# Optimization experiments

Hardware: AMD Instinct MI355X
Metric: run time of the kernel (lower is better)

Reference implementation:

```python
import jax, jax.numpy as jnp
import numpy as np

D_MODEL = 512
N_HEADS = 8
D_HEAD = D_MODEL // N_HEADS
D_FF = 2048
LN_EPS = 1e-5


def _layer_norm(x, g, b):
    mu = jnp.mean(x, axis=-1, keepdims=True)
    var = jnp.var(x, axis=-1, keepdims=True)
    return (x - mu) * jax.lax.rsqrt(var + LN_EPS) * g + b


def setup_inputs() -> dict:
    key = jax.random.key(0)
    ks = jax.random.split(key, 16)
    s_d = 1.0 / np.sqrt(D_MODEL)
    s_f = 1.0 / np.sqrt(D_FF)
    x = jax.random.normal(ks[0], (32, 512, D_MODEL), dtype=jnp.float32)
    # per-head Q/K/V linears stacked over heads: [H, D, dh] weights, [H, dh] biases
    Wq = jax.random.uniform(ks[1], (N_HEADS, D_MODEL, D_HEAD), jnp.float32, -s_d, s_d)
    bq = jax.random.uniform(ks[2], (N_HEADS, D_HEAD), jnp.float32, -s_d, s_d)
    Wk = jax.random.uniform(ks[3], (N_HEADS, D_MODEL, D_HEAD), jnp.float32, -s_d, s_d)
    bk = jax.random.uniform(ks[4], (N_HEADS, D_HEAD), jnp.float32, -s_d, s_d)
    Wv = jax.random.uniform(ks[5], (N_HEADS, D_MODEL, D_HEAD), jnp.float32, -s_d, s_d)
    bv = jax.random.uniform(ks[6], (N_HEADS, D_HEAD), jnp.float32, -s_d, s_d)
    Wo = jax.random.uniform(ks[7], (D_MODEL, D_MODEL), jnp.float32, -s_d, s_d)
    bo = jax.random.uniform(ks[8], (D_MODEL,), jnp.float32, -s_d, s_d)
    ln1_g = jnp.ones((D_MODEL,), jnp.float32)
    ln1_b = jnp.zeros((D_MODEL,), jnp.float32)
    W1 = jax.random.uniform(ks[9], (D_MODEL, D_FF), jnp.float32, -s_d, s_d)
    b1 = jax.random.uniform(ks[10], (D_FF,), jnp.float32, -s_d, s_d)
    W2 = jax.random.uniform(ks[11], (D_FF, D_MODEL), jnp.float32, -s_f, s_f)
    b2 = jax.random.uniform(ks[12], (D_MODEL,), jnp.float32, -s_f, s_f)
    ln2_g = jnp.ones((D_MODEL,), jnp.float32)
    ln2_b = jnp.zeros((D_MODEL,), jnp.float32)
    return dict(x=x, Wq=Wq, bq=bq, Wk=Wk, bk=bk, Wv=Wv, bv=bv, Wo=Wo, bo=bo,
                ln1_g=ln1_g, ln1_b=ln1_b, W1=W1, b1=b1, W2=W2, b2=b2,
                ln2_g=ln2_g, ln2_b=ln2_b)


def reference(x, Wq, bq, Wk, bk, Wv, bv, Wo, bo, ln1_g, ln1_b, W1, b1, W2, b2, ln2_g, ln2_b):
    B, T, D = x.shape
    # batched-heads Q/K/V: [B, H, T, dh]
    q = jnp.einsum('btd,hde->bhte', x, Wq) + bq[None, :, None, :]
    k = jnp.einsum('btd,hde->bhte', x, Wk) + bk[None, :, None, :]
    v = jnp.einsum('btd,hde->bhte', x, Wv) + bv[None, :, None, :]
    scale = D_HEAD ** -0.5
    scores = jnp.einsum('bhte,bhse->bhts', q, k) * scale  # [B,H,T,T]
    causal = jnp.tril(jnp.ones((T, T), dtype=bool))
    scores = jnp.where(causal[None, None], scores, -jnp.inf)
    w = jax.nn.softmax(scores, axis=-1)
    o = jnp.einsum('bhts,bhse->bhte', w, v)              # [B,H,T,dh]
    o = jnp.transpose(o, (0, 2, 1, 3)).reshape(B, T, D)   # concat heads
    attn = o @ Wo + bo
    out1 = x + _layer_norm(attn, ln1_g, ln1_b)            # post-LN on sublayer output (as in source)
    ff = jax.nn.relu(out1 @ W1 + b1) @ W2 + b2
    return out1 + _layer_norm(ff, ln2_g, ln2_b)
```

## Files before the change

### kernel.cpp

```cpp
#include <hip/hip_runtime.h>
#include <hip/hip_bf16.h>


#define D_MODEL 512
#define N_HEADS 8
#define D_HEAD 64
#define D_FF 2048
#define NROWS 16384

typedef __bf16 bf16x8 __attribute__((ext_vector_type(8)));
typedef float f32x4 __attribute__((ext_vector_type(4)));
typedef float f32x16 __attribute__((ext_vector_type(16)));

#define SWZ(x) ((x) ^ ((((x) >> 7) & 7) << 4))

static __device__ __forceinline__ ushort f2bf(float f) {
    union { float f; unsigned u; } v; v.f = f;
    unsigned r = v.u + 0x7fffu + ((v.u >> 16) & 1u);
    return (ushort)(r >> 16);
}
static __device__ __forceinline__ unsigned pack2(float lo, float hi) {
    return (unsigned)f2bf(lo) | ((unsigned)f2bf(hi) << 16);
}
static __device__ __forceinline__ float bf2f(ushort u) {
    union { unsigned u; float f; } v; v.u = (unsigned)u << 16;
    return v.f;
}
static __device__ __forceinline__ void async16(const void* g, void* l) {
    __builtin_amdgcn_global_load_lds(
        (const __attribute__((address_space(1))) void*)g,
        (__attribute__((address_space(3))) void*)l, 16, 0, 0);
}

static __device__ __forceinline__ void tile_transpose_body(
    const float* __restrict__ src, int srcldc, ushort* __restrict__ dst, int Rd,
    int r0, int c0)
{
    __shared__ float t[64][65];
    int tid = threadIdx.x;
    int lr = tid >> 4, lc4 = (tid & 15) * 4;
    #pragma unroll
    for (int i = 0; i < 4; ++i) {
        float4 v = *(const float4*)&src[(size_t)(r0 + lr + i * 16) * srcldc + c0 + lc4];
        t[lr + i * 16][lc4 + 0] = v.x;
        t[lr + i * 16][lc4 + 1] = v.y;
        t[lr + i * 16][lc4 + 2] = v.z;
        t[lr + i * 16][lc4 + 3] = v.w;
    }
    __syncthreads();
    int oc = tid >> 2, orr = (tid & 3) * 16;
    uint4 u0, u1;
    u0.x = pack2(t[orr + 0][oc],  t[orr + 1][oc]);
    u0.y = pack2(t[orr + 2][oc],  t[orr + 3][oc]);
    u0.z = pack2(t[orr + 4][oc],  t[orr + 5][oc]);
    u0.w = pack2(t[orr + 6][oc],  t[orr + 7][oc]);
    u1.x = pack2(t[orr + 8][oc],  t[orr + 9][oc]);
    u1.y = pack2(t[orr + 10][oc], t[orr + 11][oc]);
    u1.z = pack2(t[orr + 12][oc], t[orr + 13][oc]);
    u1.w = pack2(t[orr + 14][oc], t[orr + 15][oc]);
    ushort* d = dst + (size_t)(c0 + oc) * Rd + r0 + orr;
    *(uint4*)&d[0] = u0;
    *(uint4*)&d[8] = u1;
}

__global__ __launch_bounds__(256) void prep_kernel(
    const float* __restrict__ x, ushort* __restrict__ x_bf,
    const float* __restrict__ Wq, const float* __restrict__ Wk,
    const float* __restrict__ Wv, ushort* __restrict__ WpT,
    const float* __restrict__ Wo, ushort* __restrict__ WoT,
    const float* __restrict__ W1, ushort* __restrict__ W1T,
    const float* __restrict__ W2, ushort* __restrict__ W2T,
    const float* __restrict__ bq, const float* __restrict__ bk,
    const float* __restrict__ bv, float* __restrict__ bp)
{
    const int blk = blockIdx.x;
    const int tid = threadIdx.x;
    if (blk < 4096) {
        int i = blk * 256 + tid;
        const float4* s = (const float4*)x;
        float4 a = s[i * 2], b = s[i * 2 + 1];
        uint4 o;
        o.x = pack2(a.x, a.y); o.y = pack2(a.z, a.w);
        o.z = pack2(b.x, b.y); o.w = pack2(b.z, b.w);
        ((uint4*)x_bf)[i] = o;
    } else if (blk < 4288) {
        int idx = blk - 4096;
        int z = idx >> 3, y = idx & 7;
        int p = z >> 3, h = z & 7;
        const float* src = ((p == 0) ? Wq : (p == 1) ? Wk : Wv) +
                           (size_t)h * D_MODEL * D_HEAD;
        ushort* dst = WpT + (size_t)(p * D_MODEL + h * D_HEAD) * D_MODEL;
        tile_transpose_body(src, D_HEAD, dst, D_MODEL, y * 64, 0);
    } else if (blk < 4352) {
        int idx = blk - 4288;
        tile_transpose_body(Wo, 512, WoT, 512, (idx >> 3) * 64, (idx & 7) * 64);
    } else if (blk < 4608) {
        int idx = blk - 4352;
        tile_transpose_body(W1, 2048, W1T, 512, (idx >> 5) * 64, (idx & 31) * 64);
    } else if (blk < 4864) {
        int idx = blk - 4608;
        tile_transpose_body(W2, 512, W2T, 2048, (idx >> 3) * 64, (idx & 7) * 64);
    } else {
        int gid = (blk - 4864) * 256 + tid;
        if (gid < 3 * D_MODEL) {
            int p = gid / D_MODEL;
            int h = (gid % D_MODEL) / D_HEAD;
            int e = gid % D_HEAD;
            const float* bb = (p == 0) ? bq : (p == 1) ? bk : bv;
            bp[gid] = bb[h * D_HEAD + e];
        }
    }
}

template<int OMODE, bool RELU>
__global__ __launch_bounds__(512, 1) void gemm_bf16_kernel(
    const ushort* __restrict__ A, const ushort* __restrict__ BT,
    const float* __restrict__ bias, void* __restrict__ Cout,
    ushort* __restrict__ Qg, ushort* __restrict__ Kg, ushort* __restrict__ Vt,
    int M, int N, int K, int nbx)
{
    extern __shared__ __align__(16) char smem[];

    const int tid = threadIdx.x;
    const int wid = tid >> 6, l = tid & 63;
    const int wr = wid >> 1, wc = wid & 1;

    const int cpx = gridDim.x >> 3;
    const int flat = blockIdx.x;
    const int swz = (flat & 7) * cpx + (flat >> 3);
    const int bx = swz % nbx, by = swz / nbx;
    const int m0 = by * 256, n0 = bx * 128;

    const int srow = tid >> 3;
    const int sbyte = (tid & 7) * 16;
    const int ssw = sbyte ^ ((srow & 7) << 4);

    #define STAGE(t)                                                          \
    {                                                                         \
        const int kk_ = (t) * 64;                                             \
        char* dst_ = smem + ((t) & 1) * 49152;                                \
        _Pragma("unroll")                                                     \
        for (int i = 0; i < 4; ++i)                                           \
            async16((const char*)(A + (size_t)(m0 + i * 64 + srow) * K + kk_) \
                        + ssw,                                                \
                    dst_ + i * 8192 + tid * 16);                              \
        _Pragma("unroll")                                                     \
        for (int i = 0; i < 2; ++i)                                           \
            async16((const char*)(BT + (size_t)(n0 + i * 64 + srow) * K + kk_)\
                        + ssw,                                                \
                    dst_ + 32768 + i * 8192 + tid * 16);                      \
    }

    const int fl = l & 31, fh = l >> 5;
    const int frsw = (fl & 7) << 4;

    f32x16 acc[2][2] = {};

    const int T = K >> 6;
    STAGE(0);
    asm volatile("s_waitcnt vmcnt(0)" ::: "memory");
    __builtin_amdgcn_s_barrier();
    __builtin_amdgcn_sched_barrier(0);

    for (int t = 0; t < T; ++t) {
        if (t + 1 < T) STAGE(t + 1);

        const char* bufA = smem + (t & 1) * 49152;
        const char* bufB = bufA + 32768;
        #pragma unroll
        for (int ks = 0; ks < 4; ++ks) {
            const int kb = ((ks * 32 + fh * 16) ^ frsw);
            bf16x8 af[2], bfv[2];
            #pragma unroll
            for (int mi = 0; mi < 2; ++mi)
                af[mi] = *(const bf16x8*)(bufA +
                    (wr * 64 + mi * 32 + fl) * 128 + kb);
            #pragma unroll
            for (int ni = 0; ni < 2; ++ni)
                bfv[ni] = *(const bf16x8*)(bufB +
                    (wc * 64 + ni * 32 + fl) * 128 + kb);
            #pragma unroll
            for (int mi = 0; mi < 2; ++mi)
                #pragma unroll
                for (int ni = 0; ni < 2; ++ni)
                    acc[mi][ni] = __builtin_amdgcn_mfma_f32_32x32x16_bf16(
                        af[mi], bfv[ni], acc[mi][ni], 0, 0, 0);
        }

        if (t + 1 < T) {
            asm volatile("s_waitcnt vmcnt(0)" ::: "memory");
            __builtin_amdgcn_s_barrier();
            __builtin_amdgcn_sched_barrier(0);
        }
    }
    #undef STAGE

    #pragma unroll
    for (int ni = 0; ni < 2; ++ni) {
        const int c = n0 + wc * 64 + ni * 32 + fl;
        const float bvv = bias ? bias[c] : 0.f;
        #pragma unroll
        for (int mi = 0; mi < 2; ++mi) {
            const int rbase = m0 + wr * 64 + mi * 32 + (fh << 2);
            float vv[16];
            #pragma unroll
            for (int reg = 0; reg < 16; ++reg) {
                float v = acc[mi][ni][reg] + bvv;
                if (RELU) v = fmaxf(v, 0.f);
                vv[reg] = v;
            }
            if (OMODE == 1) {
                #pragma unroll
                for (int reg = 0; reg < 16; ++reg) {
                    int r = rbase + (reg & 3) + ((reg >> 2) << 3);
                    ((ushort*)Cout)[(size_t)r * N + c] = f2bf(vv[reg]);
                }
            } else {
                const int p = n0 >> 9;
                const int h = (c >> 6) & 7, e = c & 63;
                #pragma unroll
                for (int q = 0; q < 4; ++q) {
                    int r0 = rbase + (q << 3);
                    int b = r0 >> 9, t0 = r0 & 511;
                    size_t bh = (size_t)(b * 8 + h);
                    if (p == 2) {
                        uint2 pk;
                        pk.x = pack2(vv[q * 4 + 0], vv[q * 4 + 1]);
                        pk.y = pack2(vv[q * 4 + 2], vv[q * 4 + 3]);
                        *(uint2*)&Vt[bh * 32768 + (size_t)e * 512 + t0] = pk;
                    } else {
                        ushort* dst = (p == 0 ? Qg : Kg) + bh * 32768 +
                                      (size_t)t0 * 64 + e;
                        dst[0]   = f2bf(vv[q * 4 + 0]);
                        dst[64]  = f2bf(vv[q * 4 + 1]);
                        dst[128] = f2bf(vv[q * 4 + 2]);
                        dst[192] = f2bf(vv[q * 4 + 3]);
                    }
                }
            }
        }
    }
}

__global__ __launch_bounds__(256) void attn_kernel(
    const ushort* __restrict__ Qg,
    const ushort* __restrict__ Kg,
    const ushort* __restrict__ Vt,
    ushort* __restrict__ O)
{
    __shared__ __align__(16) char QP[8192];
    __shared__ __align__(16) char KB[2][8192];
    __shared__ __align__(16) char VB[2][8192];

    const int bh = blockIdx.x, qb = blockIdx.y;
    const int tid = threadIdx.x;
    const int w = tid >> 6, l = tid & 63;

    const ushort* Qb = Qg + (size_t)bh * 32768;
    const ushort* Kb = Kg + (size_t)bh * 32768;
    const ushort* Vb = Vt + (size_t)bh * 32768;

    #pragma unroll
    for (int i = 0; i < 2; ++i) {
        int Xi = i * 4096 + tid * 16;
        int row = Xi >> 7;
        int sw = SWZ(Xi) & 127;
        async16((const char*)(Qb + (size_t)(qb * 64 + row) * 64) + sw, QP + Xi);
    }
    #define STAGEKV(kt, bb)                                                     \
        { _Pragma("unroll")                                                     \
          for (int i = 0; i < 2; ++i) {                                         \
              int Xi = i * 4096 + tid * 16;                                     \
              int row = Xi >> 7;                                                \
              int sw = SWZ(Xi) & 127;                                           \
              async16((const char*)(Kb + (size_t)((kt) * 64 + row) * 64) + sw,  \
                      KB[bb] + Xi);                                             \
              async16((const char*)(Vb + (size_t)row * 512 + (kt) * 64) + sw,   \
                      VB[bb] + Xi);                                             \
          } }
    STAGEKV(0, 0);
    __syncthreads();

    bf16x8 qf[2];
    {
        int qrow = w * 16 + (l & 15);
        #pragma unroll
        for (int ks = 0; ks < 2; ++ks) {
            int X = qrow * 128 + ks * 64 + (l >> 4) * 16;
            qf[ks] = *(const bf16x8*)(QP + SWZ(X));
        }
    }

    float mrow = -INFINITY, lrow = 0.f;
    f32x4 oacc[4] = {};

    for (int kt = 0; kt <= qb; ++kt) {
        int cur = kt & 1;
        if (kt < qb) STAGEKV(kt + 1, cur ^ 1);

        f32x4 sacc[4] = {};
        #pragma unroll
        for (int ks = 0; ks < 2; ++ks) {
            #pragma unroll
            for (int mi = 0; mi < 4; ++mi) {
                int X = (mi * 16 + (l & 15)) * 128 + ks * 64 + (l >> 4) * 16;
                bf16x8 kf = *(const bf16x8*)(KB[cur] + SWZ(X));
                sacc[mi] = __builtin_amdgcn_mfma_f32_16x16x32_bf16(
                    kf, qf[ks], sacc[mi], 0, 0, 0);
            }
        }

        float sv[16];
        float tmax = -INFINITY;
        const int qrow_t = w * 16 + (l & 15);
        #pragma unroll
        for (int mi = 0; mi < 4; ++mi)
            #pragma unroll
            for (int r = 0; r < 4; ++r) {
                float s = sacc[mi][r] * 0.125f;
                if (kt == qb) {
                    int key_l = mi * 16 + (l >> 4) * 4 + r;
                    if (key_l > qrow_t) s = -INFINITY;
                }
                sv[mi * 4 + r] = s;
                tmax = fmaxf(tmax, s);
            }
        tmax = fmaxf(tmax, __shfl_xor(tmax, 16));
        tmax = fmaxf(tmax, __shfl_xor(tmax, 32));
        float mnew = fmaxf(mrow, tmax);
        float corr = __expf(mrow - mnew);
        mrow = mnew;
        float psum = 0.f;
        #pragma unroll
        for (int i = 0; i < 16; ++i) { sv[i] = __expf(sv[i] - mnew); psum += sv[i]; }
        psum += __shfl_xor(psum, 16);
        psum += __shfl_xor(psum, 32);
        lrow = lrow * corr + psum;

        #pragma unroll
        for (int mi = 0; mi < 4; ++mi) {
            uint2 pk;
            pk.x = pack2(sv[mi * 4 + 0], sv[mi * 4 + 1]);
            pk.y = pack2(sv[mi * 4 + 2], sv[mi * 4 + 3]);
            int X = qrow_t * 128 + (mi * 16 + (l >> 4) * 4) * 2;
            *(uint2*)(QP + SWZ(X)) = pk;
        }

        #pragma unroll
        for (int r = 0; r < 4; ++r) {
            float cr = __shfl(corr, (l & 48) | ((l >> 4) * 4 + r));
            #pragma unroll
            for (int n = 0; n < 4; ++n) oacc[n][r] *= cr;
        }

        #pragma unroll
        for (int ks = 0; ks < 2; ++ks) {
            int Xa = qrow_t * 128 + ks * 64 + (l >> 4) * 16;
            bf16x8 pa = *(const bf16x8*)(QP + SWZ(Xa));
            #pragma unroll
            for (int n = 0; n < 4; ++n) {
                int Xb = (n * 16 + (l & 15)) * 128 + ks * 64 + (l >> 4) * 16;
                bf16x8 vb = *(const bf16x8*)(VB[cur] + SWZ(Xb));
                oacc[n] = __builtin_amdgcn_mfma_f32_16x16x32_bf16(
                    pa, vb, oacc[n], 0, 0, 0);
            }
        }
        __syncthreads();
    }

    float linv = 1.0f / lrow;
    const int b_ = bh >> 3, h_ = bh & 7;
    #pragma unroll
    for (int r = 0; r < 4; ++r) {
        float li = __shfl(linv, (l & 48) | ((l >> 4) * 4 + r));
        int trow = qb * 64 + w * 16 + (l >> 4) * 4 + r;
        size_t obase = ((size_t)b_ * 512 + trow) * 512 + h_ * 64 + (l & 15);
        #pragma unroll
        for (int n = 0; n < 4; ++n)
            O[obase + n * 16] = f2bf(oacc[n][r] * li);
    }
}

template<bool WBF>
__global__ __launch_bounds__(256) void ln_res_kernel(
    const ushort* __restrict__ v, const float* __restrict__ res,
    const float* __restrict__ g, const float* __restrict__ bb,
    float* __restrict__ out, ushort* __restrict__ out_bf)
{
    int row  = blockIdx.x * 4 + (threadIdx.x >> 6);
    int lane = threadIdx.x & 63;
    const int c0 = lane * 8;

    uint4 vb = *(const uint4*)&v[(size_t)row * D_MODEL + c0];
    float f[8];
    f[0] = bf2f((ushort)(vb.x & 0xffff)); f[1] = bf2f((ushort)(vb.x >> 16));
    f[2] = bf2f((ushort)(vb.y & 0xffff)); f[3] = bf2f((ushort)(vb.y >> 16));
    f[4] = bf2f((ushort)(vb.z & 0xffff)); f[5] = bf2f((ushort)(vb.z >> 16));
    f[6] = bf2f((ushort)(vb.w & 0xffff)); f[7] = bf2f((ushort)(vb.w >> 16));

    float sum = 0.f, sq = 0.f;
    #pragma unroll
    for (int i = 0; i < 8; ++i) { sum += f[i]; sq += f[i] * f[i]; }
    #pragma unroll
    for (int o = 1; o < 64; o <<= 1) {
        sum += __shfl_xor(sum, o);
        sq  += __shfl_xor(sq, o);
    }
    float mu   = sum * (1.f / 512.f);
    float var  = sq * (1.f / 512.f) - mu * mu;
    float rstd = rsqrtf(var + 1e-5f);

    float4 r0 = *(const float4*)&res[(size_t)row * D_MODEL + c0];
    float4 r1 = *(const float4*)&res[(size_t)row * D_MODEL + c0 + 4];
    float4 g0 = *(const float4*)&g[c0],  g1 = *(const float4*)&g[c0 + 4];
    float4 b0 = *(const float4*)&bb[c0], b1 = *(const float4*)&bb[c0 + 4];

    float o8[8];
    o8[0] = r0.x + (f[0] - mu) * rstd * g0.x + b0.x;
    o8[1] = r0.y + (f[1] - mu) * rstd * g0.y + b0.y;
    o8[2] = r0.z + (f[2] - mu) * rstd * g0.z + b0.z;
    o8[3] = r0.w + (f[3] - mu) * rstd * g0.w + b0.w;
    o8[4] = r1.x + (f[4] - mu) * rstd * g1.x + b1.x;
    o8[5] = r1.y + (f[5] - mu) * rstd * g1.y + b1.y;
    o8[6] = r1.z + (f[6] - mu) * rstd * g1.z + b1.z;
    o8[7] = r1.w + (f[7] - mu) * rstd * g1.w + b1.w;

    float4* op = (float4*)&out[(size_t)row * D_MODEL + c0];
    op[0] = make_float4(o8[0], o8[1], o8[2], o8[3]);
    op[1] = make_float4(o8[4], o8[5], o8[6], o8[7]);
    if (WBF) {
        uint4 pk;
        pk.x = pack2(o8[0], o8[1]); pk.y = pack2(o8[2], o8[3]);
        pk.z = pack2(o8[4], o8[5]); pk.w = pack2(o8[6], o8[7]);
        *(uint4*)&out_bf[(size_t)row * D_MODEL + c0] = pk;
    }
}

extern "C" void kernel_launch(void* const* d_in, const int* in_sizes, int n_in,
                              void* d_out, int out_size, void* d_ws, size_t ws_size,
                              hipStream_t stream)
{
    const float* x     = (const float*)d_in[0];
    const float* Wq    = (const float*)d_in[1];
    const float* bq    = (const float*)d_in[2];
    const float* Wk    = (const float*)d_in[3];
    const float* bk    = (const float*)d_in[4];
    const float* Wv    = (const float*)d_in[5];
    const float* bv    = (const float*)d_in[6];
    const float* Wo    = (const float*)d_in[7];
    const float* bo    = (const float*)d_in[8];
    const float* ln1_g = (const float*)d_in[9];
    const float* ln1_b = (const float*)d_in[10];
    const float* W1    = (const float*)d_in[11];
    const float* b1    = (const float*)d_in[12];
    const float* W2    = (const float*)d_in[13];
    const float* b2    = (const float*)d_in[14];
    const float* ln2_g = (const float*)d_in[15];
    const float* ln2_b = (const float*)d_in[16];

    float* ws = (float*)d_ws;
    ushort* Qg      = (ushort*)(ws);
    ushort* Kg      = (ushort*)(ws + 4194304);
    ushort* Vt      = (ushort*)(ws + 8388608);
    ushort* O_bf    = (ushort*)(ws + 12582912);
    ushort* attn_bf = (ushort*)(ws + 16777216);
    float*  out1    = ws + 20971520;
    ushort* out1_bf = (ushort*)(ws + 29360128);
    ushort* x_bf    = (ushort*)(ws + 33554432);
    ushort* ff2_bf  = (ushort*)(ws + 37748736);
    ushort* WpT     = (ushort*)(ws + 41943040);
    ushort* WoT     = (ushort*)(ws + 42336256);
    ushort* W1T     = (ushort*)(ws + 42467328);
    ushort* W2T     = (ushort*)(ws + 42991616);
    float*  bp      = ws + 43515904;
    ushort* ff1_bf  = (ushort*)ws;

    (void)hipFuncSetAttribute(
        reinterpret_cast<const void*>(&gemm_bf16_kernel<2, false>),
        hipFuncAttributeMaxDynamicSharedMemorySize, 98304);
    (void)hipFuncSetAttribute(
        reinterpret_cast<const void*>(&gemm_bf16_kernel<1, false>),
        hipFuncAttributeMaxDynamicSharedMemorySize, 98304);
    (void)hipFuncSetAttribute(
        reinterpret_cast<const void*>(&gemm_bf16_kernel<1, true>),
        hipFuncAttributeMaxDynamicSharedMemorySize, 98304);

    prep_kernel<<<dim3(4870), 256, 0, stream>>>(
        x, x_bf, Wq, Wk, Wv, WpT, Wo, WoT, W1, W1T, W2, W2T, bq, bk, bv, bp);

    gemm_bf16_kernel<2, false><<<dim3(768), 512, 98304, stream>>>(
        x_bf, WpT, bp, nullptr, Qg, Kg, Vt, NROWS, 1536, 512, 12);

    attn_kernel<<<dim3(256, 8), 256, 0, stream>>>(Qg, Kg, Vt, O_bf);

    gemm_bf16_kernel<1, false><<<dim3(256), 512, 98304, stream>>>(
        O_bf, WoT, bo, attn_bf, nullptr, nullptr, nullptr, NROWS, 512, 512, 4);

    ln_res_kernel<true><<<dim3(NROWS / 4), 256, 0, stream>>>(
        attn_bf, x, ln1_g, ln1_b, out1, out1_bf);

    gemm_bf16_kernel<1, true><<<dim3(1024), 512, 98304, stream>>>(
        out1_bf, W1T, b1, ff1_bf, nullptr, nullptr, nullptr, NROWS, 2048, 512, 16);

    gemm_bf16_kernel<1, false><<<dim3(256), 512, 98304, stream>>>(
        ff1_bf, W2T, b2, ff2_bf, nullptr, nullptr, nullptr, NROWS, 512, 2048, 4);

    ln_res_kernel<false><<<dim3(NROWS / 4), 256, 0, stream>>>(
        ff2_bf, out1, ln2_g, ln2_b, (float*)d_out, nullptr);
}
```

Baseline: 211.7 us.

## Shrink GEMM tiles to 128x128 single-buffered blocks for higher occupancy

The bf16 GEMM changes from 512-thread blocks with 256x128 tiles and double-buffered 96KB LDS to 256-thread blocks with 128x128 tiles and a single 32KB LDS buffer, doubling grid sizes. Launch bounds now target 4 blocks per CU, so latency is hidden by occupancy instead of software prefetch. The trade is that each k-step now waits on its own load with no overlap inside a block, and each output element does more global operand traffic.

```diff
diff --git a/kernel.cpp b/kernel.cpp
--- a/kernel.cpp
+++ b/kernel.cpp
@@ -113,7 +113,7 @@
 }
 
 template<int OMODE, bool RELU>
-__global__ __launch_bounds__(512, 1) void gemm_bf16_kernel(
+__global__ __launch_bounds__(256, 4) void gemm_bf16_kernel(
     const ushort* __restrict__ A, const ushort* __restrict__ BT,
     const float* __restrict__ bias, void* __restrict__ Cout,
     ushort* __restrict__ Qg, ushort* __restrict__ Kg, ushort* __restrict__ Vt,
@@ -129,7 +129,7 @@
     const int flat = blockIdx.x;
     const int swz = (flat & 7) * cpx + (flat >> 3);
     const int bx = swz % nbx, by = swz / nbx;
-    const int m0 = by * 256, n0 = bx * 128;
+    const int m0 = by * 128, n0 = bx * 128;
 
     const int srow = tid >> 3;
     const int sbyte = (tid & 7) * 16;
@@ -138,17 +138,15 @@
     #define STAGE(t)                                                          \
     {                                                                         \
         const int kk_ = (t) * 64;                                             \
-        char* dst_ = smem + ((t) & 1) * 49152;                                \
         _Pragma("unroll")                                                     \
-        for (int i = 0; i < 4; ++i)                                           \
-            async16((const char*)(A + (size_t)(m0 + i * 64 + srow) * K + kk_) \
+        for (int i = 0; i < 4; ++i) {                                         \
+            async16((const char*)(A + (size_t)(m0 + i * 32 + srow) * K + kk_) \
                         + ssw,                                                \
-                    dst_ + i * 8192 + tid * 16);                              \
-        _Pragma("unroll")                                                     \
-        for (int i = 0; i < 2; ++i)                                           \
-            async16((const char*)(BT + (size_t)(n0 + i * 64 + srow) * K + kk_)\
+                    smem + i * 4096 + tid * 16);                              \
+            async16((const char*)(BT + (size_t)(n0 + i * 32 + srow) * K + kk_)\
                         + ssw,                                                \
-                    dst_ + 32768 + i * 8192 + tid * 16);                      \
+                    smem + 16384 + i * 4096 + tid * 16);                      \
+        }                                                                     \
     }
 
     const int fl = l & 31, fh = l >> 5;
@@ -157,16 +155,14 @@
     f32x16 acc[2][2] = {};
 
     const int T = K >> 6;
-    STAGE(0);
-    asm volatile("s_waitcnt vmcnt(0)" ::: "memory");
-    __builtin_amdgcn_s_barrier();
-    __builtin_amdgcn_sched_barrier(0);
-
     for (int t = 0; t < T; ++t) {
-        if (t + 1 < T) STAGE(t + 1);
-
-        const char* bufA = smem + (t & 1) * 49152;
-        const char* bufB = bufA + 32768;
+        STAGE(t);
+        asm volatile("s_waitcnt vmcnt(0)" ::: "memory");
+        __builtin_amdgcn_s_barrier();
+        __builtin_amdgcn_sched_barrier(0);
+
+        const char* bufA = smem;
+        const char* bufB = smem + 16384;
         #pragma unroll
         for (int ks = 0; ks < 4; ++ks) {
             const int kb = ((ks * 32 + fh * 16) ^ frsw);
@@ -186,12 +182,7 @@
                     acc[mi][ni] = __builtin_amdgcn_mfma_f32_32x32x16_bf16(
                         af[mi], bfv[ni], acc[mi][ni], 0, 0, 0);
         }
-
-        if (t + 1 < T) {
-            asm volatile("s_waitcnt vmcnt(0)" ::: "memory");
-            __builtin_amdgcn_s_barrier();
-            __builtin_amdgcn_sched_barrier(0);
-        }
+        __builtin_amdgcn_s_barrier();
     }
     #undef STAGE
 
@@ -475,34 +466,24 @@
     float*  bp      = ws + 43515904;
     ushort* ff1_bf  = (ushort*)ws;
 
-    (void)hipFuncSetAttribute(
-        reinterpret_cast<const void*>(&gemm_bf16_kernel<2, false>),
-        hipFuncAttributeMaxDynamicSharedMemorySize, 98304);
-    (void)hipFuncSetAttribute(
-        reinterpret_cast<const void*>(&gemm_bf16_kernel<1, false>),
-        hipFuncAttributeMaxDynamicSharedMemorySize, 98304);
-    (void)hipFuncSetAttribute(
-        reinterpret_cast<const void*>(&gemm_bf16_kernel<1, true>),
-        hipFuncAttributeMaxDynamicSharedMemorySize, 98304);
-
     prep_kernel<<<dim3(4870), 256, 0, stream>>>(
         x, x_bf, Wq, Wk, Wv, WpT, Wo, WoT, W1, W1T, W2, W2T, bq, bk, bv, bp);
 
-    gemm_bf16_kernel<2, false><<<dim3(768), 512, 98304, stream>>>(
+    gemm_bf16_kernel<2, false><<<dim3(1536), 256, 32768, stream>>>(
         x_bf, WpT, bp, nullptr, Qg, Kg, Vt, NROWS, 1536, 512, 12);
 
     attn_kernel<<<dim3(256, 8), 256, 0, stream>>>(Qg, Kg, Vt, O_bf);
 
-    gemm_bf16_kernel<1, false><<<dim3(256), 512, 98304, stream>>>(
+    gemm_bf16_kernel<1, false><<<dim3(512), 256, 32768, stream>>>(
         O_bf, WoT, bo, attn_bf, nullptr, nullptr, nullptr, NROWS, 512, 512, 4);
 
     ln_res_kernel<true><<<dim3(NROWS / 4), 256, 0, stream>>>(
         attn_bf, x, ln1_g, ln1_b, out1, out1_bf);
 
-    gemm_bf16_kernel<1, true><<<dim3(1024), 512, 98304, stream>>>(
+    gemm_bf16_kernel<1, true><<<dim3(2048), 256, 32768, stream>>>(
         out1_bf, W1T, b1, ff1_bf, nullptr, nullptr, nullptr, NROWS, 2048, 512, 16);
 
-    gemm_bf16_kernel<1, false><<<dim3(256), 512, 98304, stream>>>(
+    gemm_bf16_kernel<1, false><<<dim3(512), 256, 32768, stream>>>(
         ff1_bf, W2T, b2, ff2_bf, nullptr, nullptr, nullptr, NROWS, 512, 2048, 4);
 
     ln_res_kernel<false><<<dim3(NROWS / 4), 256, 0, stream>>>(
```

New measurement: 218.6 us. +3.3%, slower.

## Fuse output-projection and FFN2 GEMMs with LayerNorm and residual epilogue

Applied to the files above, without the earlier changes.

Adds a GEMM kernel where each block computes a full 64x512 row tile, so each block can reduce the LayerNorm statistics across its 8 waves through shared memory. Residual add and affine transform are applied in the epilogue. This replaces two GEMM launches plus two separate LN kernels, removing the bf16 round-trip of the intermediate activations and two launches. In exchange it uses 144KB of shared memory, one block per CU and a 64-row tile, which may reduce GEMM efficiency. The epilogue stores are scalar and strided, and the LN input now stays fp32 where it was previously bf16-rounded.

```diff
diff --git a/kernel.cpp b/kernel.cpp
--- a/kernel.cpp
+++ b/kernel.cpp
@@ -242,6 +242,146 @@
     }
 }
 
+template<bool WB>
+__global__ __launch_bounds__(512, 1) void gemm_ln_kernel(
+    const ushort* __restrict__ A, const ushort* __restrict__ BT,
+    const float* __restrict__ bias, const float* __restrict__ res,
+    const float* __restrict__ g, const float* __restrict__ beta,
+    float* __restrict__ outf, ushort* __restrict__ outb, int K)
+{
+    extern __shared__ __align__(16) char smem[];
+
+    const int tid = threadIdx.x;
+    const int wid = tid >> 6, l = tid & 63;
+    const int wn = wid;
+
+    const int cpx = gridDim.x >> 3;
+    const int flat = blockIdx.x;
+    const int swz = (flat & 7) * cpx + (flat >> 3);
+    const int m0 = swz * 64;
+
+    const int srow = tid >> 3;
+    const int ssw = ((tid & 7) * 16) ^ ((srow & 7) << 4);
+
+    #define STAGE2(t)                                                         \
+    {                                                                         \
+        const int kk_ = (t) * 64;                                             \
+        char* dst_ = smem + ((t) & 1) * 73728;                                \
+        async16((const char*)(A + (size_t)(m0 + srow) * K + kk_) + ssw,       \
+                dst_ + tid * 16);                                             \
+        _Pragma("unroll")                                                     \
+        for (int i = 0; i < 8; ++i)                                           \
+            async16((const char*)(BT + (size_t)(i * 64 + srow) * K + kk_)     \
+                        + ssw,                                                \
+                    dst_ + 8192 + i * 8192 + tid * 16);                       \
+    }
+
+    const int fl = l & 31, fh = l >> 5;
+    const int frsw = (fl & 7) << 4;
+
+    f32x16 acc[2][2] = {};
+
+    const int T = K >> 6;
+    STAGE2(0);
+    asm volatile("s_waitcnt vmcnt(0)" ::: "memory");
+    __builtin_amdgcn_s_barrier();
+    __builtin_amdgcn_sched_barrier(0);
+
+    for (int t = 0; t < T; ++t) {
+        if (t + 1 < T) STAGE2(t + 1);
+
+        const char* bufA = smem + (t & 1) * 73728;
+        const char* bufB = bufA + 8192;
+        #pragma unroll
+        for (int ks = 0; ks < 4; ++ks) {
+            const int kb = ((ks * 32 + fh * 16) ^ frsw);
+            bf16x8 af[2], bfv[2];
+            #pragma unroll
+            for (int mi = 0; mi < 2; ++mi)
+                af[mi] = *(const bf16x8*)(bufA + (mi * 32 + fl) * 128 + kb);
+            #pragma unroll
+            for (int ni = 0; ni < 2; ++ni)
+                bfv[ni] = *(const bf16x8*)(bufB +
+                    (wn * 64 + ni * 32 + fl) * 128 + kb);
+            #pragma unroll
+            for (int mi = 0; mi < 2; ++mi)
+                #pragma unroll
+                for (int ni = 0; ni < 2; ++ni)
+                    acc[mi][ni] = __builtin_amdgcn_mfma_f32_32x32x16_bf16(
+                        af[mi], bfv[ni], acc[mi][ni], 0, 0, 0);
+        }
+
+        if (t + 1 < T) {
+            asm volatile("s_waitcnt vmcnt(0)" ::: "memory");
+            __builtin_amdgcn_s_barrier();
+            __builtin_amdgcn_sched_barrier(0);
+        }
+    }
+    #undef STAGE2
+
+    #pragma unroll
+    for (int ni = 0; ni < 2; ++ni) {
+        const float bvv = bias[wn * 64 + ni * 32 + fl];
+        #pragma unroll
+        for (int mi = 0; mi < 2; ++mi)
+            #pragma unroll
+            for (int reg = 0; reg < 16; ++reg)
+                acc[mi][ni][reg] += bvv;
+    }
+
+    float* part = (float*)smem;
+    __syncthreads();
+    #pragma unroll
+    for (int mi = 0; mi < 2; ++mi)
+        #pragma unroll
+        for (int reg = 0; reg < 16; ++reg) {
+            int r = mi * 32 + (reg & 3) + ((reg >> 2) << 3) + (fh << 2);
+            float s = acc[mi][0][reg] + acc[mi][1][reg];
+            float q = acc[mi][0][reg] * acc[mi][0][reg] +
+                      acc[mi][1][reg] * acc[mi][1][reg];
+            #pragma unroll
+            for (int o = 1; o < 32; o <<= 1) {
+                s += __shfl_xor(s, o);
+                q += __shfl_xor(q, o);
+            }
+            if (fl == 0) {
+                part[(wid * 64 + r) * 2 + 0] = s;
+                part[(wid * 64 + r) * 2 + 1] = q;
+            }
+        }
+    __syncthreads();
+    float2* mrstd = (float2*)(smem + 4096);
+    if (tid < 64) {
+        float s = 0.f, q = 0.f;
+        #pragma unroll
+        for (int w = 0; w < 8; ++w) {
+            s += part[(w * 64 + tid) * 2 + 0];
+            q += part[(w * 64 + tid) * 2 + 1];
+        }
+        float mu  = s * (1.f / 512.f);
+        float var = q * (1.f / 512.f) - mu * mu;
+        mrstd[tid] = make_float2(mu, rsqrtf(var + 1e-5f));
+    }
+    __syncthreads();
+
+    #pragma unroll
+    for (int ni = 0; ni < 2; ++ni) {
+        const int c = wn * 64 + ni * 32 + fl;
+        const float gc = g[c], bc = beta[c];
+        #pragma unroll
+        for (int mi = 0; mi < 2; ++mi)
+            #pragma unroll
+            for (int reg = 0; reg < 16; ++reg) {
+                int rl = mi * 32 + (reg & 3) + ((reg >> 2) << 3) + (fh << 2);
+                float2 ms = mrstd[rl];
+                size_t off = (size_t)(m0 + rl) * 512 + c;
+                float o = res[off] + (acc[mi][ni][reg] - ms.x) * ms.y * gc + bc;
+                outf[off] = o;
+                if (WB) outb[off] = f2bf(o);
+            }
+    }
+}
+
 __global__ __launch_bounds__(256) void attn_kernel(
     const ushort* __restrict__ Qg,
     const ushort* __restrict__ Kg,
@@ -378,61 +518,6 @@
         #pragma unroll
         for (int n = 0; n < 4; ++n)
             O[obase + n * 16] = f2bf(oacc[n][r] * li);
-    }
-}
-
-template<bool WBF>
-__global__ __launch_bounds__(256) void ln_res_kernel(
-    const ushort* __restrict__ v, const float* __restrict__ res,
-    const float* __restrict__ g, const float* __restrict__ bb,
-    float* __restrict__ out, ushort* __restrict__ out_bf)
-{
-    int row  = blockIdx.x * 4 + (threadIdx.x >> 6);
-    int lane = threadIdx.x & 63;
-    const int c0 = lane * 8;
-
-    uint4 vb = *(const uint4*)&v[(size_t)row * D_MODEL + c0];
-    float f[8];
-    f[0] = bf2f((ushort)(vb.x & 0xffff)); f[1] = bf2f((ushort)(vb.x >> 16));
-    f[2] = bf2f((ushort)(vb.y & 0xffff)); f[3] = bf2f((ushort)(vb.y >> 16));
-    f[4] = bf2f((ushort)(vb.z & 0xffff)); f[5] = bf2f((ushort)(vb.z >> 16));
-    f[6] = bf2f((ushort)(vb.w & 0xffff)); f[7] = bf2f((ushort)(vb.w >> 16));
-
-    float sum = 0.f, sq = 0.f;
-    #pragma unroll
-    for (int i = 0; i < 8; ++i) { sum += f[i]; sq += f[i] * f[i]; }
-    #pragma unroll
-    for (int o = 1; o < 64; o <<= 1) {
-        sum += __shfl_xor(sum, o);
-        sq  += __shfl_xor(sq, o);
-    }
-    float mu   = sum * (1.f / 512.f);
-    float var  = sq * (1.f / 512.f) - mu * mu;
-    float rstd = rsqrtf(var + 1e-5f);
-
-    float4 r0 = *(const float4*)&res[(size_t)row * D_MODEL + c0];
-    float4 r1 = *(const float4*)&res[(size_t)row * D_MODEL + c0 + 4];
-    float4 g0 = *(const float4*)&g[c0],  g1 = *(const float4*)&g[c0 + 4];
-    float4 b0 = *(const float4*)&bb[c0], b1 = *(const float4*)&bb[c0 + 4];
-
-    float o8[8];
-    o8[0] = r0.x + (f[0] - mu) * rstd * g0.x + b0.x;
-    o8[1] = r0.y + (f[1] - mu) * rstd * g0.y + b0.y;
-    o8[2] = r0.z + (f[2] - mu) * rstd * g0.z + b0.z;
-    o8[3] = r0.w + (f[3] - mu) * rstd * g0.w + b0.w;
-    o8[4] = r1.x + (f[4] - mu) * rstd * g1.x + b1.x;
-    o8[5] = r1.y + (f[5] - mu) * rstd * g1.y + b1.y;
-    o8[6] = r1.z + (f[6] - mu) * rstd * g1.z + b1.z;
-    o8[7] = r1.w + (f[7] - mu) * rstd * g1.w + b1.w;
-
-    float4* op = (float4*)&out[(size_t)row * D_MODEL + c0];
-    op[0] = make_float4(o8[0], o8[1], o8[2], o8[3]);
-    op[1] = make_float4(o8[4], o8[5], o8[6], o8[7]);
-    if (WBF) {
-        uint4 pk;
-        pk.x = pack2(o8[0], o8[1]); pk.y = pack2(o8[2], o8[3]);
-        pk.z = pack2(o8[4], o8[5]); pk.w = pack2(o8[6], o8[7]);
-        *(uint4*)&out_bf[(size_t)row * D_MODEL + c0] = pk;
     }
 }
 
@@ -463,11 +548,9 @@
     ushort* Kg      = (ushort*)(ws + 4194304);
     ushort* Vt      = (ushort*)(ws + 8388608);
     ushort* O_bf    = (ushort*)(ws + 12582912);
-    ushort* attn_bf = (ushort*)(ws + 16777216);
     float*  out1    = ws + 20971520;
     ushort* out1_bf = (ushort*)(ws + 29360128);
     ushort* x_bf    = (ushort*)(ws + 33554432);
-    ushort* ff2_bf  = (ushort*)(ws + 37748736);
     ushort* WpT     = (ushort*)(ws + 41943040);
     ushort* WoT     = (ushort*)(ws + 42336256);
     ushort* W1T     = (ushort*)(ws + 42467328);
@@ -479,11 +562,14 @@
         reinterpret_cast<const void*>(&gemm_bf16_kernel<2, false>),
         hipFuncAttributeMaxDynamicSharedMemorySize, 98304);
     (void)hipFuncSetAttribute(
-        reinterpret_cast<const void*>(&gemm_bf16_kernel<1, false>),
+        reinterpret_cast<const void*>(&gemm_bf16_kernel<1, true>),
         hipFuncAttributeMaxDynamicSharedMemorySize, 98304);
     (void)hipFuncSetAttribute(
-        reinterpret_cast<const void*>(&gemm_bf16_kernel<1, true>),
-        hipFuncAttributeMaxDynamicSharedMemorySize, 98304);
+        reinterpret_cast<const void*>(&gemm_ln_kernel<true>),
+        hipFuncAttributeMaxDynamicSharedMemorySize, 147456);
+    (void)hipFuncSetAttribute(
+        reinterpret_cast<const void*>(&gemm_ln_kernel<false>),
+        hipFuncAttributeMaxDynamicSharedMemorySize, 147456);
 
     prep_kernel<<<dim3(4870), 256, 0, stream>>>(
         x, x_bf, Wq, Wk, Wv, WpT, Wo, WoT, W1, W1T, W2, W2T, bq, bk, bv, bp);
@@ -493,18 +579,12 @@
 
     attn_kernel<<<dim3(256, 8), 256, 0, stream>>>(Qg, Kg, Vt, O_bf);
 
-    gemm_bf16_kernel<1, false><<<dim3(256), 512, 98304, stream>>>(
-        O_bf, WoT, bo, attn_bf, nullptr, nullptr, nullptr, NROWS, 512, 512, 4);
-
-    ln_res_kernel<true><<<dim3(NROWS / 4), 256, 0, stream>>>(
-        attn_bf, x, ln1_g, ln1_b, out1, out1_bf);
+    gemm_ln_kernel<true><<<dim3(256), 512, 147456, stream>>>(
+        O_bf, WoT, bo, x, ln1_g, ln1_b, out1, out1_bf, 512);
 
     gemm_bf16_kernel<1, true><<<dim3(1024), 512, 98304, stream>>>(
         out1_bf, W1T, b1, ff1_bf, nullptr, nullptr, nullptr, NROWS, 2048, 512, 16);
 
-    gemm_bf16_kernel<1, false><<<dim3(256), 512, 98304, stream>>>(
-        ff1_bf, W2T, b2, ff2_bf, nullptr, nullptr, nullptr, NROWS, 512, 2048, 4);
-
-    ln_res_kernel<false><<<dim3(NROWS / 4), 256, 0, stream>>>(
-        ff2_bf, out1, ln2_g, ln2_b, (float*)d_out, nullptr);
-}
+    gemm_ln_kernel<false><<<dim3(256), 512, 147456, stream>>>(
+        ff1_bf, W2T, b2, out1, ln2_g, ln2_b, (float*)d_out, nullptr, 2048);
+}
```

After: 227.5 us. +7.5%, slower.
